# Kernel optimization log

Measured on AMD Instinct MI355X. Metric: run time of the kernel, lower is better.

Reference implementation:

```python
import jax, jax.numpy as jnp
import numpy as np

BN_EPS = 1e-5


def binarize(x):
    # Deterministic sign binarization to {-1, +1} (binarization mode 1).
    return jnp.where(x >= 0, 1.0, -1.0).astype(x.dtype)


def setup_inputs() -> dict:
    key = jax.random.key(0)
    k = jax.random.split(key, 4)
    N, Cin, Cout, H, W, K = 16, 64, 64, 256, 256, 3
    x = jax.random.normal(k[0], (N, Cin, H, W), dtype=jnp.float32)
    w = jax.random.normal(k[1], (Cout, Cin, K, K), dtype=jnp.float32) * 0.1
    b = jax.random.normal(k[2], (Cout,), dtype=jnp.float32) * 0.1
    gamma = jnp.ones((Cout,), dtype=jnp.float32)
    beta = jnp.zeros((Cout,), dtype=jnp.float32)
    running_mean = jax.random.normal(k[3], (Cout,), dtype=jnp.float32) * 0.1
    running_var = jax.random.uniform(jax.random.fold_in(key, 7), (Cout,), dtype=jnp.float32, minval=0.5, maxval=1.5)
    return {"x": x, "w": w, "b": b, "gamma": gamma, "beta": beta,
            "running_mean": running_mean, "running_var": running_var}


def reference(x, w, b, gamma, beta, running_mean, running_var):
    # binarize activations and weights to +-1
    xb = binarize(x)
    wb = binarize(w)
    # 3x3 conv, stride 1, padding 1, dilation 1, NCHW/OIHW
    y = jax.lax.conv_general_dilated(
        xb, wb,
        window_strides=(1, 1),
        padding=((1, 1), (1, 1)),
        dimension_numbers=("NCHW", "OIHW", "NCHW"),
    ) + b[None, :, None, None]
    # ReLU
    y = jnp.maximum(y, 0.0)
    # Dropout2d in eval mode is identity.
    # BatchNorm2d in eval mode: use running stats, affine=True.
    inv = gamma * jax.lax.rsqrt(running_var + BN_EPS)
    y = y * inv[None, :, None, None] + (beta - running_mean * inv)[None, :, None, None]
    return y
```

## Files before the change

### kernel.cpp

```cpp
#include <hip/hip_runtime.h>
#include <stdint.h>

#define NB 16
#define CC 64
#define HH 256
#define WW 256
#define HP 258
#define WP 258

__global__ __launch_bounds__(256) void pack_w_kernel(const float* __restrict__ w,
                                                     uint64_t* __restrict__ pW) {
    int widx = (blockIdx.x * 256 + threadIdx.x) >> 6;
    int lane = threadIdx.x & 63;
    if (widx >= CC * 9) return;
    int o = widx / 9;
    int t = widx % 9;
    float v = w[(size_t)o * (CC * 9) + (size_t)lane * 9 + t];
    unsigned long long m = __ballot(v < 0.0f);
    if (lane == 0) pW[widx] = m;
}

__global__ __launch_bounds__(256) void pack_x_kernel(const float* __restrict__ x,
                                                     uint64_t* __restrict__ pX) {
    int n = blockIdx.y;
    if (blockIdx.x == 0) {
        for (int r = threadIdx.x; r < 1028; r += 256) {
            size_t base = (size_t)n * HP * WP;
            size_t off;
            if (r < 258) off = (size_t)r;
            else if (r < 516) off = (size_t)257 * WP + (r - 258);
            else {
                int rr = r - 516;
                off = (size_t)(1 + (rr >> 1)) * WP + ((rr & 1) ? 257 : 0);
            }
            pX[base + off] = 0;
        }
    }
    int g = blockIdx.x * 256 + threadIdx.x;
    const float4* xv = (const float4*)x;
    uint64_t b0 = 0, b1 = 0, b2 = 0, b3 = 0;
#pragma unroll 16
    for (int c = 0; c < CC; ++c) {
        float4 v = xv[((size_t)(n * CC + c) << 14) + g];
        b0 |= (uint64_t)(v.x < 0.0f) << c;
        b1 |= (uint64_t)(v.y < 0.0f) << c;
        b2 |= (uint64_t)(v.z < 0.0f) << c;
        b3 |= (uint64_t)(v.w < 0.0f) << c;
    }
    int px = g << 2;
    int h = px >> 8;
    int w = px & 255;
    uint64_t* dst = pX + ((size_t)n * HP + (h + 1)) * WP + (w + 1);
    dst[0] = b0; dst[1] = b1; dst[2] = b2; dst[3] = b3;
}

__global__ __launch_bounds__(256, 4) void bconv_kernel(const uint64_t* __restrict__ pX,
                                                       const uint64_t* __restrict__ pW,
                                                       const float* __restrict__ bias,
                                                       const float* __restrict__ gamma,
                                                       const float* __restrict__ beta,
                                                       const float* __restrict__ rmean,
                                                       const float* __restrict__ rvar,
                                                       float* __restrict__ out) {
    __shared__ uint64_t sq[CC][9];
    __shared__ int si[CC][8];
    __shared__ float sf[CC][3];

    int tid = threadIdx.x;
    if (tid < CC) {
        int o = tid;
        int ct[9];
#pragma unroll
        for (int t = 0; t < 9; ++t) {
            uint64_t q = pW[o * 9 + t];
            sq[o][t] = q;
            ct[t] = 64 - 2 * __popcll(q);
        }
        si[o][0] = ct[0] + ct[1] + ct[2];
        si[o][1] = ct[6] + ct[7] + ct[8];
        si[o][2] = ct[0] + ct[3] + ct[6];
        si[o][3] = ct[2] + ct[5] + ct[8];
        si[o][4] = ct[0]; si[o][5] = ct[2]; si[o][6] = ct[6]; si[o][7] = ct[8];
        float inv = gamma[o] / sqrtf(rvar[o] + 1e-5f);
        sf[o][0] = bias[o];
        sf[o][1] = inv;
        sf[o][2] = beta[o] - rmean[o] * inv;
    }

    int blk = blockIdx.x;
    int n = blk >> 6;
    int hq = blk & 63;
    int l = tid & 63;
    int wid = tid >> 6;
    int h = hq * 4 + wid;

    uint64_t xw[3][6];
    const uint64_t* rowp = pX + ((size_t)n * HP + h) * WP + 4 * l;
#pragma unroll
    for (int r = 0; r < 3; ++r) {
        const ulonglong2* p2 = (const ulonglong2*)(rowp + (size_t)r * WP);
        ulonglong2 a = p2[0], b = p2[1], c = p2[2];
        xw[r][0] = a.x; xw[r][1] = a.y; xw[r][2] = b.x;
        xw[r][3] = b.y; xw[r][4] = c.x; xw[r][5] = c.y;
    }

    __syncthreads();

    bool isL = (l == 0), isR = (l == 63);
    bool isT = (h == 0), isB = (h == 255);
    float4* out4 = (float4*)out;
    size_t obase = ((size_t)(n * CC) << 14) + (size_t)h * 64 + l;

#pragma unroll 2
    for (int o = 0; o < CC; ++o) {
        uint64_t q0 = sq[o][0], q1 = sq[o][1], q2 = sq[o][2];
        uint64_t q3 = sq[o][3], q4 = sq[o][4], q5 = sq[o][5];
        uint64_t q6 = sq[o][6], q7 = sq[o][7], q8 = sq[o][8];
        int hcorr = 0, cL = si[o][2], cR = si[o][3];
        if (isT) { hcorr += si[o][0]; cL -= si[o][4]; cR -= si[o][5]; }
        if (isB) { hcorr += si[o][1]; cL -= si[o][6]; cR -= si[o][7]; }
        float bo = sf[o][0], inv = sf[o][1], addc = sf[o][2];

        float4 res;
        float* resp = (float*)&res;
#pragma unroll
        for (int j = 0; j < 4; ++j) {
            int p = __popcll(xw[0][j] ^ q0) + __popcll(xw[0][j + 1] ^ q1) + __popcll(xw[0][j + 2] ^ q2)
                  + __popcll(xw[1][j] ^ q3) + __popcll(xw[1][j + 1] ^ q4) + __popcll(xw[1][j + 2] ^ q5)
                  + __popcll(xw[2][j] ^ q6) + __popcll(xw[2][j + 1] ^ q7) + __popcll(xw[2][j + 2] ^ q8);
            int corr = hcorr;
            if (j == 0 && isL) corr += cL;
            if (j == 3 && isR) corr += cR;
            float yf = (float)(576 - 2 * p - corr) + bo;
            yf = fmaxf(yf, 0.0f);
            resp[j] = fmaf(yf, inv, addc);
        }
        out4[obase + ((size_t)o << 14)] = res;
    }
}

extern "C" void kernel_launch(void* const* d_in, const int* in_sizes, int n_in,
                              void* d_out, int out_size, void* d_ws, size_t ws_size,
                              hipStream_t stream) {
    const float* x     = (const float*)d_in[0];
    const float* w     = (const float*)d_in[1];
    const float* bias  = (const float*)d_in[2];
    const float* gamma = (const float*)d_in[3];
    const float* beta  = (const float*)d_in[4];
    const float* rmean = (const float*)d_in[5];
    const float* rvar  = (const float*)d_in[6];
    float* out = (float*)d_out;

    uint64_t* pX = (uint64_t*)d_ws;
    size_t pXwords = (size_t)NB * HP * WP;
    uint64_t* pW = pX + pXwords;

    pack_w_kernel<<<(CC * 9 + 3) / 4, 256, 0, stream>>>(w, pW);
    pack_x_kernel<<<dim3(64, NB), 256, 0, stream>>>(x, pX);
    bconv_kernel<<<NB * 64, 256, 0, stream>>>(pX, pW, bias, gamma, beta, rmean, rvar, out);
}
```

Before: 514.7 us.

## Fuse activation bit-packing into the binary conv kernel via shared-memory tile

Removes the separate pack_x kernel and its global packed-activation buffer. Each 512-thread block now packs its 8 output rows plus a halo directly from the float input into a shared-memory tile, then runs the XOR-popcount convolution from that tile. This avoids writing and re-reading the packed workspace and one kernel launch. In exchange it re-reads halo rows (about 25% extra input traffic), serialises pack and compute within a block, and lowers the block count, which may reduce latency hiding.

```diff
diff --git a/kernel.cpp b/kernel.cpp
--- a/kernel.cpp
+++ b/kernel.cpp
@@ -5,7 +5,6 @@
 #define CC 64
 #define HH 256
 #define WW 256
-#define HP 258
 #define WP 258
 
 __global__ __launch_bounds__(256) void pack_w_kernel(const float* __restrict__ w,
@@ -20,41 +19,7 @@
     if (lane == 0) pW[widx] = m;
 }
 
-__global__ __launch_bounds__(256) void pack_x_kernel(const float* __restrict__ x,
-                                                     uint64_t* __restrict__ pX) {
-    int n = blockIdx.y;
-    if (blockIdx.x == 0) {
-        for (int r = threadIdx.x; r < 1028; r += 256) {
-            size_t base = (size_t)n * HP * WP;
-            size_t off;
-            if (r < 258) off = (size_t)r;
-            else if (r < 516) off = (size_t)257 * WP + (r - 258);
-            else {
-                int rr = r - 516;
-                off = (size_t)(1 + (rr >> 1)) * WP + ((rr & 1) ? 257 : 0);
-            }
-            pX[base + off] = 0;
-        }
-    }
-    int g = blockIdx.x * 256 + threadIdx.x;
-    const float4* xv = (const float4*)x;
-    uint64_t b0 = 0, b1 = 0, b2 = 0, b3 = 0;
-#pragma unroll 16
-    for (int c = 0; c < CC; ++c) {
-        float4 v = xv[((size_t)(n * CC + c) << 14) + g];
-        b0 |= (uint64_t)(v.x < 0.0f) << c;
-        b1 |= (uint64_t)(v.y < 0.0f) << c;
-        b2 |= (uint64_t)(v.z < 0.0f) << c;
-        b3 |= (uint64_t)(v.w < 0.0f) << c;
-    }
-    int px = g << 2;
-    int h = px >> 8;
-    int w = px & 255;
-    uint64_t* dst = pX + ((size_t)n * HP + (h + 1)) * WP + (w + 1);
-    dst[0] = b0; dst[1] = b1; dst[2] = b2; dst[3] = b3;
-}
-
-__global__ __launch_bounds__(256, 4) void bconv_kernel(const uint64_t* __restrict__ pX,
+__global__ __launch_bounds__(512, 4) void fused_kernel(const float* __restrict__ x,
                                                        const uint64_t* __restrict__ pW,
                                                        const float* __restrict__ bias,
                                                        const float* __restrict__ gamma,
@@ -62,11 +27,16 @@
                                                        const float* __restrict__ rmean,
                                                        const float* __restrict__ rvar,
                                                        float* __restrict__ out) {
+    __shared__ uint64_t tile[10][WP];
     __shared__ uint64_t sq[CC][9];
     __shared__ int si[CC][8];
     __shared__ float sf[CC][3];
 
+    int blk = blockIdx.x;
+    int n = blk >> 5;
+    int h0 = (blk & 31) << 3;
     int tid = threadIdx.x;
+
     if (tid < CC) {
         int o = tid;
         int ct[9];
@@ -87,29 +57,46 @@
         sf[o][2] = beta[o] - rmean[o] * inv;
     }
 
-    int blk = blockIdx.x;
-    int n = blk >> 6;
-    int hq = blk & 63;
+    const float4* xv = (const float4*)x;
+    for (int i = tid; i < 640; i += 512) {
+        int r = i >> 6;
+        int g = i & 63;
+        int xr = h0 + r - 1;
+        uint64_t b0 = 0, b1 = 0, b2 = 0, b3 = 0;
+        if (xr >= 0 && xr < HH) {
+            size_t base = (((size_t)n * CC) << 14) + ((size_t)xr << 6) + g;
+#pragma unroll 16
+            for (int c = 0; c < CC; ++c) {
+                float4 v = xv[base + ((size_t)c << 14)];
+                b0 |= (uint64_t)(v.x < 0.0f) << c;
+                b1 |= (uint64_t)(v.y < 0.0f) << c;
+                b2 |= (uint64_t)(v.z < 0.0f) << c;
+                b3 |= (uint64_t)(v.w < 0.0f) << c;
+            }
+        }
+        uint64_t* dst = &tile[r][4 * g + 1];
+        dst[0] = b0; dst[1] = b1; dst[2] = b2; dst[3] = b3;
+    }
+    if (tid < 20) tile[tid >> 1][(tid & 1) * 257] = 0;
+
+    __syncthreads();
+
     int l = tid & 63;
-    int wid = tid >> 6;
-    int h = hq * 4 + wid;
+    int wv = tid >> 6;
+    int h = h0 + wv;
 
     uint64_t xw[3][6];
-    const uint64_t* rowp = pX + ((size_t)n * HP + h) * WP + 4 * l;
 #pragma unroll
-    for (int r = 0; r < 3; ++r) {
-        const ulonglong2* p2 = (const ulonglong2*)(rowp + (size_t)r * WP);
-        ulonglong2 a = p2[0], b = p2[1], c = p2[2];
-        xw[r][0] = a.x; xw[r][1] = a.y; xw[r][2] = b.x;
-        xw[r][3] = b.y; xw[r][4] = c.x; xw[r][5] = c.y;
+    for (int rr = 0; rr < 3; ++rr) {
+        const uint64_t* rp = &tile[wv + rr][4 * l];
+#pragma unroll
+        for (int k = 0; k < 6; ++k) xw[rr][k] = rp[k];
     }
-
-    __syncthreads();
 
     bool isL = (l == 0), isR = (l == 63);
     bool isT = (h == 0), isB = (h == 255);
     float4* out4 = (float4*)out;
-    size_t obase = ((size_t)(n * CC) << 14) + (size_t)h * 64 + l;
+    size_t obase = (((size_t)n * CC) << 14) + (size_t)h * 64 + l;
 
 #pragma unroll 2
     for (int o = 0; o < CC; ++o) {
@@ -151,11 +138,8 @@
     const float* rvar  = (const float*)d_in[6];
     float* out = (float*)d_out;
 
-    uint64_t* pX = (uint64_t*)d_ws;
-    size_t pXwords = (size_t)NB * HP * WP;
-    uint64_t* pW = pX + pXwords;
+    uint64_t* pW = (uint64_t*)d_ws;
 
     pack_w_kernel<<<(CC * 9 + 3) / 4, 256, 0, stream>>>(w, pW);
-    pack_x_kernel<<<dim3(64, NB), 256, 0, stream>>>(x, pX);
-    bconv_kernel<<<NB * 64, 256, 0, stream>>>(pX, pW, bias, gamma, beta, rmean, rvar, out);
+    fused_kernel<<<NB * 32, 512, 0, stream>>>(x, pW, bias, gamma, beta, rmean, rvar, out);
 }
```

After: 515.3 us. Within noise of the previous version (+0.1%).
